# Performance work log

Hardware: AMD Instinct MI355X
Metric: run time of the kernel (lower is better)

The kernel has to match this reference:

```python
import jax, jax.numpy as jnp
import numpy as np

N_NODES = 100000
N_EDGES = 1200000
D = 64          # node_feat_size
G_FEAT = 128    # graph_feat_size
N_GRAPHS = 256
N_TASKS = 1


def setup_inputs() -> dict:
    key = jax.random.key(0)
    ks = jax.random.split(key, 12)
    node_feats = jax.random.normal(ks[0], (N_NODES, D), dtype=jnp.float32)
    edge_feats = jax.random.normal(ks[1], (N_EDGES, 8), dtype=jnp.float32)
    src = jax.random.randint(ks[2], (N_EDGES,), 0, N_NODES, dtype=jnp.int64 if jax.config.read('jax_enable_x64') else jnp.int32)
    dst = jax.random.randint(ks[3], (N_EDGES,), 0, N_NODES, dtype=src.dtype)
    graph_ids = jnp.sort(jax.random.randint(ks[4], (N_NODES,), 0, N_GRAPHS, dtype=src.dtype))
    s = 1.0 / np.sqrt(D)
    W_gcn = jax.random.uniform(ks[5], (D, D), minval=-s, maxval=s, dtype=jnp.float32)
    b_gcn = jnp.zeros((D,), jnp.float32)
    W_res = jax.random.uniform(ks[6], (D, D), minval=-s, maxval=s, dtype=jnp.float32)
    b_res = jnp.zeros((D,), jnp.float32)
    W_in = jax.random.uniform(ks[7], (D, D), minval=-s, maxval=s, dtype=jnp.float32)
    b_in = jnp.zeros((D,), jnp.float32)
    W_out = jax.random.uniform(ks[8], (D, G_FEAT), minval=-s, maxval=s, dtype=jnp.float32)
    b_out = jnp.zeros((G_FEAT,), jnp.float32)
    sp = 1.0 / np.sqrt(G_FEAT)
    W_pred = jax.random.uniform(ks[9], (G_FEAT, N_TASKS), minval=-sp, maxval=sp, dtype=jnp.float32)
    b_pred = jnp.zeros((N_TASKS,), jnp.float32)
    return dict(node_feats=node_feats, edge_feats=edge_feats, src=src, dst=dst,
                graph_ids=graph_ids, W_gcn=W_gcn, b_gcn=b_gcn, W_res=W_res, b_res=b_res,
                W_in=W_in, b_in=b_in, W_out=W_out, b_out=b_out, W_pred=W_pred, b_pred=b_pred)


def reference(node_feats, edge_feats, src, dst, graph_ids,
              W_gcn, b_gcn, W_res, b_res, W_in, b_in, W_out, b_out, W_pred, b_pred):
    # --- GCNLayer (GraphConv norm='none', activation=relu, residual=True) ---
    # message passing: copy src features, sum at dst (no normalization)
    agg = jax.ops.segment_sum(node_feats[src], dst, num_segments=N_NODES)  # [N, D]
    h = jax.nn.relu(agg @ W_gcn + b_gcn)                                   # graph_conv output
    h = h + jax.nn.relu(node_feats @ W_res + b_res)                        # residual branch
    # --- MLPNodeReadout (mode='sum') ---
    h = jax.nn.relu(h @ W_in + b_in)      # [N, D]
    h = h @ W_out + b_out                 # [N, G_FEAT]
    g_feats = jax.ops.segment_sum(h, graph_ids, num_segments=N_GRAPHS)  # [G, G_FEAT]
    # --- predict ---
    out = (g_feats @ W_pred + b_pred).reshape(-1)  # [G * n_tasks]
    return out
```

## Files before the change

kernel.cpp:

```cpp
#include <hip/hip_runtime.h>

typedef __attribute__((ext_vector_type(8))) __bf16 bf16x8;
typedef __attribute__((ext_vector_type(4))) float f32x4;

union Frag { unsigned short u[8]; bf16x8 b; };

__device__ __forceinline__ unsigned short rne_bf16(float x) {
    unsigned int u = __float_as_uint(x);
    return (unsigned short)((u + 0x7fffu + ((u >> 16) & 1u)) >> 16);
}
__device__ __forceinline__ float bf16_to_f(unsigned short h) {
    return __uint_as_float(((unsigned int)h) << 16);
}

#define MFMA16 __builtin_amdgcn_mfma_f32_16x16x32_bf16
#define BCAP 8192

__global__ void prep_kernel(const float* __restrict__ nf,
                            const float* __restrict__ Wg, const float* __restrict__ Wr,
                            const float* __restrict__ Wi, const float* __restrict__ Wo,
                            const float* __restrict__ bo, const float* __restrict__ Wp,
                            const float* __restrict__ bp,
                            unsigned short* __restrict__ nfb,
                            unsigned short* __restrict__ wfrag, float* __restrict__ wfold,
                            float* __restrict__ c0, float* __restrict__ out,
                            int* __restrict__ gcursor, int out_size, int nNodes) {
    int t = blockIdx.x * blockDim.x + threadIdx.x;
    int nth = gridDim.x * blockDim.x;
    const float4* nf4 = (const float4*)nf;
    ushort4* nfb4 = (ushort4*)nfb;
    int nQ = nNodes * 16;
    for (int i = t; i < nQ; i += nth) {
        float4 v = nf4[i];
        ushort4 o;
        o.x = rne_bf16(v.x); o.y = rne_bf16(v.y);
        o.z = rne_bf16(v.z); o.w = rne_bf16(v.w);
        nfb4[i] = o;
    }
    const float* Ws[3] = {Wg, Wr, Wi};
    for (int idx = t; idx < 3 * 2 * 2 * 4 * 64 * 8; idx += nth) {
        int j = idx & 7, lane = (idx >> 3) & 63, nt = (idx >> 9) & 3;
        int kt = (idx >> 11) & 1, part = (idx >> 12) & 1, mat = idx >> 13;
        int k = kt * 32 + ((lane >> 4) << 3) + j;
        int n = nt * 16 + (lane & 15);
        float w = Ws[mat][k * 64 + n];
        unsigned short hi = rne_bf16(w);
        wfrag[idx] = (part == 0) ? hi : rne_bf16(w - bf16_to_f(hi));
    }
    if (t < 64) {
        float s = 0.f;
        for (int j = 0; j < 128; ++j) s += Wo[t * 128 + j] * Wp[j];
        wfold[t] = s;
    }
    if (t == 0) {
        float s = 0.f;
        for (int j = 0; j < 128; ++j) s += bo[j] * Wp[j];
        c0[0] = s;
    }
    if (t < out_size) out[t] = bp[0];
    if (t < 256) gcursor[t] = 0;
}

__global__ __launch_bounds__(256) void bin_kernel(
    const int* __restrict__ src, const int* __restrict__ dst,
    int* __restrict__ gcursor, int* __restrict__ binned, int nE, int nb) {
    __shared__ int lhist[256];
    __shared__ int lbase[256];
    __shared__ int lpos[256];
    int t = threadIdx.x;
    for (int i = t; i < nb; i += 256) { lhist[i] = 0; lpos[i] = 0; }
    __syncthreads();
    int base = blockIdx.x * 4096;
    int end = min(base + 4096, nE);
    for (int e = base + t; e < end; e += 256)
        atomicAdd(&lhist[dst[e] >> 9], 1);
    __syncthreads();
    for (int i = t; i < nb; i += 256) {
        int c = lhist[i];
        lbase[i] = c ? atomicAdd(&gcursor[i], c) : 0;
    }
    __syncthreads();
    for (int e = base + t; e < end; e += 256) {
        int d = dst[e];
        int b = d >> 9;
        int p = atomicAdd(&lpos[b], 1);
        int gp = lbase[b] + p;
        if (gp < BCAP) binned[b * BCAP + gp] = (src[e] << 9) | (d & 511);
    }
}

__global__ __launch_bounds__(1024) void seg_kernel(
    int* __restrict__ binned, const int* __restrict__ gcursor,
    int2* __restrict__ nodeTab, int nNodes) {
    __shared__ int eL[BCAP];
    __shared__ int deg[512];
    __shared__ int scanb[512];
    __shared__ int cur[512];
    const int b = blockIdx.x, t = threadIdx.x;
    const int cnt = min(gcursor[b], BCAP);
    if (t < 512) deg[t] = 0;
    __syncthreads();
    for (int i = t; i < cnt; i += 1024) {
        int p = binned[b * BCAP + i];
        eL[i] = p;
        atomicAdd(&deg[p & 511], 1);
    }
    __syncthreads();
    if (t < 512) scanb[t] = deg[t];
    __syncthreads();
    for (int s = 1; s < 512; s <<= 1) {
        int v = 0;
        if (t < 512 && t >= s) v = scanb[t - s];
        __syncthreads();
        if (t < 512) scanb[t] += v;
        __syncthreads();
    }
    if (t < 512) {
        int excl = scanb[t] - deg[t];
        cur[t] = excl;
        int node = b * 512 + t;
        if (node < nNodes) nodeTab[node] = make_int2(b * BCAP + excl, deg[t]);
    }
    __syncthreads();
    for (int i = t; i < cnt; i += 1024) {
        int p = eL[i];
        int pos = atomicAdd(&cur[p & 511], 1);
        binned[b * BCAP + pos] = p >> 9;
    }
}

__global__ __launch_bounds__(256) void gather_kernel(
    const unsigned short* __restrict__ nfb, const int2* __restrict__ nodeTab,
    const int* __restrict__ srcs, unsigned short* __restrict__ aggb, int nNodes) {
    int wid = blockIdx.x * 4 + (threadIdx.x >> 6);
    if (wid >= nNodes) return;
    int lane = threadIdx.x & 63;
    int half = lane >> 5;
    int cp = lane & 31;
    int2 sd = nodeTab[wid];
    int base = sd.x, d = sd.y;
    const ushort2* nfb2 = (const ushort2*)nfb;
    float ax = 0.f, ay = 0.f;
    int k = half;
    for (; k + 8 <= d; k += 8) {
        int s0 = srcs[base + k],     s1 = srcs[base + k + 2];
        int s2 = srcs[base + k + 4], s3 = srcs[base + k + 6];
        ushort2 v0 = nfb2[(long)s0 * 32 + cp];
        ushort2 v1 = nfb2[(long)s1 * 32 + cp];
        ushort2 v2 = nfb2[(long)s2 * 32 + cp];
        ushort2 v3 = nfb2[(long)s3 * 32 + cp];
        ax += (bf16_to_f(v0.x) + bf16_to_f(v1.x)) + (bf16_to_f(v2.x) + bf16_to_f(v3.x));
        ay += (bf16_to_f(v0.y) + bf16_to_f(v1.y)) + (bf16_to_f(v2.y) + bf16_to_f(v3.y));
    }
    for (; k < d; k += 2) {
        int s = srcs[base + k];
        ushort2 v = nfb2[(long)s * 32 + cp];
        ax += bf16_to_f(v.x); ay += bf16_to_f(v.y);
    }
    ax += __shfl_xor(ax, 32, 64);
    ay += __shfl_xor(ay, 32, 64);
    if (half == 0) {
        ushort2 o; o.x = rne_bf16(ax); o.y = rne_bf16(ay);
        ((ushort2*)aggb)[(long)wid * 32 + cp] = o;
    }
}

__global__ __launch_bounds__(256) void mlp_kernel(
    const unsigned short* __restrict__ aggb, const unsigned short* __restrict__ nfb,
    const int* __restrict__ gids, const unsigned short* __restrict__ wfrag,
    const float* __restrict__ bg, const float* __restrict__ br,
    const float* __restrict__ bi, const float* __restrict__ wfold,
    const float* __restrict__ c0p, float* __restrict__ out, int nTiles) {
    __shared__ float hs_all[4][32 * 68];
    const int wave = threadIdx.x >> 6, lane = threadIdx.x & 63;
    const int wid = blockIdx.x * 4 + wave;
    if (wid >= nTiles) return;
    float* hs = hs_all[wave];
    const int base = wid * 32;
    const int mrow = lane & 15, quad = lane >> 4;

    Frag aA[2][2], aN[2][2];
    #pragma unroll
    for (int rt = 0; rt < 2; ++rt) {
        const unsigned short* rowA = aggb + (long)(base + rt * 16 + mrow) * 64;
        const unsigned short* rowN = nfb  + (long)(base + rt * 16 + mrow) * 64;
        #pragma unroll
        for (int kt = 0; kt < 2; ++kt) {
            aA[rt][kt].b = *(const bf16x8*)(rowA + kt * 32 + quad * 8);
            aN[rt][kt].b = *(const bf16x8*)(rowN + kt * 32 + quad * 8);
        }
    }

    const unsigned short* wl0 = wfrag + lane * 8;
    auto WF = [&](int mat, int part, int kt, int nt) -> bf16x8 {
        return *(const bf16x8*)(wl0 + (size_t)((((mat * 2 + part) * 2 + kt) * 4 + nt) * 64) * 8);
    };

    f32x4 accA[2][4], accR[2][4];
    #pragma unroll
    for (int rt = 0; rt < 2; ++rt)
        #pragma unroll
        for (int nt = 0; nt < 4; ++nt) {
            accA[rt][nt] = (f32x4){0.f, 0.f, 0.f, 0.f};
            accR[rt][nt] = (f32x4){0.f, 0.f, 0.f, 0.f};
        }
    #pragma unroll
    for (int nt = 0; nt < 4; ++nt)
        #pragma unroll
        for (int kt = 0; kt < 2; ++kt) {
            bf16x8 gh = WF(0, 0, kt, nt), gl = WF(0, 1, kt, nt);
            bf16x8 rh = WF(1, 0, kt, nt), rl = WF(1, 1, kt, nt);
            #pragma unroll
            for (int rt = 0; rt < 2; ++rt) {
                accA[rt][nt] = MFMA16(aA[rt][kt].b, gh, accA[rt][nt], 0, 0, 0);
                accA[rt][nt] = MFMA16(aA[rt][kt].b, gl, accA[rt][nt], 0, 0, 0);
                accR[rt][nt] = MFMA16(aN[rt][kt].b, rh, accR[rt][nt], 0, 0, 0);
                accR[rt][nt] = MFMA16(aN[rt][kt].b, rl, accR[rt][nt], 0, 0, 0);
            }
        }

    #pragma unroll
    for (int nt = 0; nt < 4; ++nt) {
        float bgv = bg[nt * 16 + mrow], brv = br[nt * 16 + mrow];
        #pragma unroll
        for (int rt = 0; rt < 2; ++rt)
            #pragma unroll
            for (int r = 0; r < 4; ++r) {
                float h = fmaxf(accA[rt][nt][r] + bgv, 0.f)
                        + fmaxf(accR[rt][nt][r] + brv, 0.f);
                hs[(rt * 16 + quad * 4 + r) * 68 + nt * 16 + mrow] = h;
            }
    }
    __builtin_amdgcn_wave_barrier();

    Frag aH[2][2];
    #pragma unroll
    for (int rt = 0; rt < 2; ++rt)
        #pragma unroll
        for (int kt = 0; kt < 2; ++kt) {
            const float* hp = hs + (rt * 16 + mrow) * 68 + kt * 32 + quad * 8;
            float4 v0 = *(const float4*)hp;
            float4 v1 = *(const float4*)(hp + 4);
            aH[rt][kt].u[0] = rne_bf16(v0.x); aH[rt][kt].u[1] = rne_bf16(v0.y);
            aH[rt][kt].u[2] = rne_bf16(v0.z); aH[rt][kt].u[3] = rne_bf16(v0.w);
            aH[rt][kt].u[4] = rne_bf16(v1.x); aH[rt][kt].u[5] = rne_bf16(v1.y);
            aH[rt][kt].u[6] = rne_bf16(v1.z); aH[rt][kt].u[7] = rne_bf16(v1.w);
        }
    f32x4 accH[2][4];
    #pragma unroll
    for (int rt = 0; rt < 2; ++rt)
        #pragma unroll
        for (int nt = 0; nt < 4; ++nt)
            accH[rt][nt] = (f32x4){0.f, 0.f, 0.f, 0.f};
    #pragma unroll
    for (int nt = 0; nt < 4; ++nt)
        #pragma unroll
        for (int kt = 0; kt < 2; ++kt) {
            bf16x8 ih = WF(2, 0, kt, nt), il = WF(2, 1, kt, nt);
            #pragma unroll
            for (int rt = 0; rt < 2; ++rt) {
                accH[rt][nt] = MFMA16(aH[rt][kt].b, ih, accH[rt][nt], 0, 0, 0);
                accH[rt][nt] = MFMA16(aH[rt][kt].b, il, accH[rt][nt], 0, 0, 0);
            }
        }

    float p[2][4];
    #pragma unroll
    for (int rt = 0; rt < 2; ++rt)
        #pragma unroll
        for (int r = 0; r < 4; ++r) p[rt][r] = 0.f;
    #pragma unroll
    for (int nt = 0; nt < 4; ++nt) {
        float biv = bi[nt * 16 + mrow], wfv = wfold[nt * 16 + mrow];
        #pragma unroll
        for (int rt = 0; rt < 2; ++rt)
            #pragma unroll
            for (int r = 0; r < 4; ++r)
                p[rt][r] += fmaxf(accH[rt][nt][r] + biv, 0.f) * wfv;
    }
    #pragma unroll
    for (int m = 1; m <= 8; m <<= 1)
        #pragma unroll
        for (int rt = 0; rt < 2; ++rt)
            #pragma unroll
            for (int r = 0; r < 4; ++r)
                p[rt][r] += __shfl_xor(p[rt][r], m, 64);
    const float c0 = c0p[0];
    #pragma unroll
    for (int rt = 0; rt < 2; ++rt)
        #pragma unroll
        for (int r = 0; r < 4; ++r) p[rt][r] += c0;

    int gself = gids[base + (lane & 31)];
    int g0 = __shfl(gself, 0, 64);
    if (__all(gself == g0)) {
        float pv = 0.f;
        if (mrow == 0) {
            #pragma unroll
            for (int rt = 0; rt < 2; ++rt)
                #pragma unroll
                for (int r = 0; r < 4; ++r) pv += p[rt][r];
        }
        pv += __shfl_xor(pv, 16, 64);
        pv += __shfl_xor(pv, 32, 64);
        if (lane == 0) atomicAdd(out + g0, pv);
    } else if (mrow == 0) {
        #pragma unroll
        for (int rt = 0; rt < 2; ++rt)
            #pragma unroll
            for (int r = 0; r < 4; ++r)
                atomicAdd(out + gids[base + rt * 16 + quad * 4 + r], p[rt][r]);
    }
}

extern "C" void kernel_launch(void* const* d_in, const int* in_sizes, int n_in,
                              void* d_out, int out_size, void* d_ws, size_t ws_size,
                              hipStream_t stream) {
    const float* node_feats = (const float*)d_in[0];
    const int* src  = (const int*)d_in[2];
    const int* dst  = (const int*)d_in[3];
    const int* gids = (const int*)d_in[4];
    const float* Wg = (const float*)d_in[5];
    const float* bg = (const float*)d_in[6];
    const float* Wr = (const float*)d_in[7];
    const float* br = (const float*)d_in[8];
    const float* Wi = (const float*)d_in[9];
    const float* bi = (const float*)d_in[10];
    const float* Wo = (const float*)d_in[11];
    const float* bo = (const float*)d_in[12];
    const float* Wp = (const float*)d_in[13];
    const float* bp = (const float*)d_in[14];
    float* out = (float*)d_out;

    const int nNodes = in_sizes[0] / 64;
    const int nE = in_sizes[2];
    const int nb = (nNodes + 511) / 512;

    int* gcursor = (int*)d_ws;
    int* binned  = gcursor + 256;
    int2* nodeTab = (int2*)(binned + (size_t)nb * BCAP);
    unsigned short* nfb  = (unsigned short*)(nodeTab + nNodes);
    unsigned short* aggb = nfb + (size_t)nNodes * 64;
    unsigned short* wfrag = aggb + (size_t)nNodes * 64;
    float* wfold = (float*)(wfrag + 3 * 2 * 2 * 4 * 64 * 8);
    float* c0 = wfold + 64;

    prep_kernel<<<2048, 256, 0, stream>>>(node_feats, Wg, Wr, Wi, Wo, bo, Wp, bp,
                                          nfb, wfrag, wfold, c0, out, gcursor,
                                          out_size, nNodes);
    bin_kernel<<<(nE + 4095) / 4096, 256, 0, stream>>>(src, dst, gcursor, binned, nE, nb);
    seg_kernel<<<nb, 1024, 0, stream>>>(binned, gcursor, nodeTab, nNodes);
    gather_kernel<<<(nNodes + 3) / 4, 256, 0, stream>>>(nfb, nodeTab, binned, aggb, nNodes);

    const int nTiles = (nNodes + 31) / 32;
    mlp_kernel<<<(nTiles + 3) / 4, 256, 0, stream>>>(aggb, nfb, gids, wfrag,
        bg, br, bi, wfold, c0, out, nTiles);
}
```

Before: 232.2 us.

## Fuse prep and binning into one kernel with finer 128-node buckets

Merges the bf16 conversion/weight prep kernel with the edge binning kernel into a single launch, with separate block ranges doing each job concurrently. Bucket size drops from 512 to 128 nodes (782 buckets, capacity 2048 each), so seg_kernel runs more, smaller 256-thread blocks with a shorter scan and less LDS. The cursor reset moves to a memset. This removes a launch and lets binning overlap with the conversion, but the smaller bucket capacity leaves less slack for overflow and the prep side now runs on fewer blocks.

```diff
diff --git a/kernel.cpp b/kernel.cpp
--- a/kernel.cpp
+++ b/kernel.cpp
@@ -14,23 +14,53 @@
 }
 
 #define MFMA16 __builtin_amdgcn_mfma_f32_16x16x32_bf16
-#define BCAP 8192
-
-__global__ void prep_kernel(const float* __restrict__ nf,
-                            const float* __restrict__ Wg, const float* __restrict__ Wr,
-                            const float* __restrict__ Wi, const float* __restrict__ Wo,
-                            const float* __restrict__ bo, const float* __restrict__ Wp,
-                            const float* __restrict__ bp,
-                            unsigned short* __restrict__ nfb,
-                            unsigned short* __restrict__ wfrag, float* __restrict__ wfold,
-                            float* __restrict__ c0, float* __restrict__ out,
-                            int* __restrict__ gcursor, int out_size, int nNodes) {
-    int t = blockIdx.x * blockDim.x + threadIdx.x;
-    int nth = gridDim.x * blockDim.x;
+#define BSH 7
+#define BNODES 128
+#define BCAP 2048
+#define BINCHUNK 4096
+#define NWFRAG (3 * 2 * 2 * 4 * 64 * 8)
+
+__global__ __launch_bounds__(256) void prepbin_kernel(
+    const float* __restrict__ nf, const int* __restrict__ src,
+    const int* __restrict__ dst,
+    const float* __restrict__ Wg, const float* __restrict__ Wr,
+    const float* __restrict__ Wi, const float* __restrict__ Wo,
+    const float* __restrict__ bo, const float* __restrict__ Wp,
+    const float* __restrict__ bp,
+    unsigned short* __restrict__ nfb, unsigned short* __restrict__ wfrag,
+    float* __restrict__ wfold, float* __restrict__ c0, float* __restrict__ out,
+    int* __restrict__ gcursor, int* __restrict__ binned,
+    int nBin, int nE, int nb, int out_size, int nNodes) {
+    __shared__ int lhist[800], lbase[800], lpos[800];
+    const int t = threadIdx.x;
+    if ((int)blockIdx.x < nBin) {
+        for (int i = t; i < nb; i += 256) { lhist[i] = 0; lpos[i] = 0; }
+        __syncthreads();
+        const int e0 = blockIdx.x * BINCHUNK;
+        const int e1 = min(e0 + BINCHUNK, nE);
+        for (int e = e0 + t; e < e1; e += 256)
+            atomicAdd(&lhist[dst[e] >> BSH], 1);
+        __syncthreads();
+        for (int i = t; i < nb; i += 256) {
+            int c = lhist[i];
+            lbase[i] = c ? atomicAdd(&gcursor[i], c) : 0;
+        }
+        __syncthreads();
+        for (int e = e0 + t; e < e1; e += 256) {
+            int d = dst[e];
+            int bkt = d >> BSH;
+            int p = atomicAdd(&lpos[bkt], 1);
+            int gp = lbase[bkt] + p;
+            if (gp < BCAP) binned[bkt * BCAP + gp] = (src[e] << BSH) | (d & (BNODES - 1));
+        }
+        return;
+    }
+    const int tp = ((int)blockIdx.x - nBin) * 256 + t;
+    const int nth = ((int)gridDim.x - nBin) * 256;
     const float4* nf4 = (const float4*)nf;
     ushort4* nfb4 = (ushort4*)nfb;
-    int nQ = nNodes * 16;
-    for (int i = t; i < nQ; i += nth) {
+    const int nQ = nNodes * 16;
+    for (int i = tp; i < nQ; i += nth) {
         float4 v = nf4[i];
         ushort4 o;
         o.x = rne_bf16(v.x); o.y = rne_bf16(v.y);
@@ -38,7 +68,7 @@
         nfb4[i] = o;
     }
     const float* Ws[3] = {Wg, Wr, Wi};
-    for (int idx = t; idx < 3 * 2 * 2 * 4 * 64 * 8; idx += nth) {
+    for (int idx = tp; idx < NWFRAG; idx += nth) {
         int j = idx & 7, lane = (idx >> 3) & 63, nt = (idx >> 9) & 3;
         int kt = (idx >> 11) & 1, part = (idx >> 12) & 1, mat = idx >> 13;
         int k = kt * 32 + ((lane >> 4) << 3) + j;
@@ -47,85 +77,55 @@
         unsigned short hi = rne_bf16(w);
         wfrag[idx] = (part == 0) ? hi : rne_bf16(w - bf16_to_f(hi));
     }
-    if (t < 64) {
+    if (tp < 64) {
         float s = 0.f;
-        for (int j = 0; j < 128; ++j) s += Wo[t * 128 + j] * Wp[j];
-        wfold[t] = s;
-    }
-    if (t == 0) {
+        for (int j = 0; j < 128; ++j) s += Wo[tp * 128 + j] * Wp[j];
+        wfold[tp] = s;
+    }
+    if (tp == 0) {
         float s = 0.f;
         for (int j = 0; j < 128; ++j) s += bo[j] * Wp[j];
         c0[0] = s;
     }
-    if (t < out_size) out[t] = bp[0];
-    if (t < 256) gcursor[t] = 0;
-}
-
-__global__ __launch_bounds__(256) void bin_kernel(
-    const int* __restrict__ src, const int* __restrict__ dst,
-    int* __restrict__ gcursor, int* __restrict__ binned, int nE, int nb) {
-    __shared__ int lhist[256];
-    __shared__ int lbase[256];
-    __shared__ int lpos[256];
-    int t = threadIdx.x;
-    for (int i = t; i < nb; i += 256) { lhist[i] = 0; lpos[i] = 0; }
-    __syncthreads();
-    int base = blockIdx.x * 4096;
-    int end = min(base + 4096, nE);
-    for (int e = base + t; e < end; e += 256)
-        atomicAdd(&lhist[dst[e] >> 9], 1);
-    __syncthreads();
-    for (int i = t; i < nb; i += 256) {
-        int c = lhist[i];
-        lbase[i] = c ? atomicAdd(&gcursor[i], c) : 0;
-    }
-    __syncthreads();
-    for (int e = base + t; e < end; e += 256) {
-        int d = dst[e];
-        int b = d >> 9;
-        int p = atomicAdd(&lpos[b], 1);
-        int gp = lbase[b] + p;
-        if (gp < BCAP) binned[b * BCAP + gp] = (src[e] << 9) | (d & 511);
-    }
-}
-
-__global__ __launch_bounds__(1024) void seg_kernel(
+    if (tp < out_size) out[tp] = bp[0];
+}
+
+__global__ __launch_bounds__(256) void seg_kernel(
     int* __restrict__ binned, const int* __restrict__ gcursor,
     int2* __restrict__ nodeTab, int nNodes) {
     __shared__ int eL[BCAP];
-    __shared__ int deg[512];
-    __shared__ int scanb[512];
-    __shared__ int cur[512];
+    __shared__ int deg[BNODES], sc[BNODES], cur[BNODES];
     const int b = blockIdx.x, t = threadIdx.x;
     const int cnt = min(gcursor[b], BCAP);
-    if (t < 512) deg[t] = 0;
+    if (t < BNODES) deg[t] = 0;
     __syncthreads();
-    for (int i = t; i < cnt; i += 1024) {
+    for (int i = t; i < cnt; i += 256) {
         int p = binned[b * BCAP + i];
         eL[i] = p;
-        atomicAdd(&deg[p & 511], 1);
+        atomicAdd(&deg[p & (BNODES - 1)], 1);
     }
     __syncthreads();
-    if (t < 512) scanb[t] = deg[t];
+    if (t < BNODES) sc[t] = deg[t];
     __syncthreads();
-    for (int s = 1; s < 512; s <<= 1) {
+    #pragma unroll
+    for (int s = 1; s < BNODES; s <<= 1) {
         int v = 0;
-        if (t < 512 && t >= s) v = scanb[t - s];
-        __syncthreads();
-        if (t < 512) scanb[t] += v;
-        __syncthreads();
-    }
-    if (t < 512) {
-        int excl = scanb[t] - deg[t];
+        if (t < BNODES && t >= s) v = sc[t - s];
+        __syncthreads();
+        if (t < BNODES) sc[t] += v;
+        __syncthreads();
+    }
+    if (t < BNODES) {
+        int excl = sc[t] - deg[t];
         cur[t] = excl;
-        int node = b * 512 + t;
+        int node = b * BNODES + t;
         if (node < nNodes) nodeTab[node] = make_int2(b * BCAP + excl, deg[t]);
     }
     __syncthreads();
-    for (int i = t; i < cnt; i += 1024) {
+    for (int i = t; i < cnt; i += 256) {
         int p = eL[i];
-        int pos = atomicAdd(&cur[p & 511], 1);
-        binned[b * BCAP + pos] = p >> 9;
+        int pos = atomicAdd(&cur[p & (BNODES - 1)], 1);
+        binned[b * BCAP + pos] = p >> BSH;
     }
 }
 
@@ -334,22 +334,26 @@
 
     const int nNodes = in_sizes[0] / 64;
     const int nE = in_sizes[2];
-    const int nb = (nNodes + 511) / 512;
+    const int nb = (nNodes + BNODES - 1) / BNODES;
 
     int* gcursor = (int*)d_ws;
-    int* binned  = gcursor + 256;
+    int* binned  = gcursor + 1024;
     int2* nodeTab = (int2*)(binned + (size_t)nb * BCAP);
     unsigned short* nfb  = (unsigned short*)(nodeTab + nNodes);
     unsigned short* aggb = nfb + (size_t)nNodes * 64;
     unsigned short* wfrag = aggb + (size_t)nNodes * 64;
-    float* wfold = (float*)(wfrag + 3 * 2 * 2 * 4 * 64 * 8);
+    float* wfold = (float*)(wfrag + NWFRAG);
     float* c0 = wfold + 64;
 
-    prep_kernel<<<2048, 256, 0, stream>>>(node_feats, Wg, Wr, Wi, Wo, bo, Wp, bp,
-                                          nfb, wfrag, wfold, c0, out, gcursor,
-                                          out_size, nNodes);
-    bin_kernel<<<(nE + 4095) / 4096, 256, 0, stream>>>(src, dst, gcursor, binned, nE, nb);
-    seg_kernel<<<nb, 1024, 0, stream>>>(binned, gcursor, nodeTab, nNodes);
+    hipMemsetAsync(gcursor, 0, 1024 * sizeof(int), stream);
+
+    const int nBin = (nE + BINCHUNK - 1) / BINCHUNK;
+    prepbin_kernel<<<nBin + 512, 256, 0, stream>>>(
+        node_feats, src, dst, Wg, Wr, Wi, Wo, bo, Wp, bp,
+        nfb, wfrag, wfold, c0, out, gcursor, binned,
+        nBin, nE, nb, out_size, nNodes);
+
+    seg_kernel<<<nb, 256, 0, stream>>>(binned, gcursor, nodeTab, nNodes);
     gather_kernel<<<(nNodes + 3) / 4, 256, 0, stream>>>(nfb, nodeTab, binned, aggb, nNodes);
 
     const int nTiles = (nNodes + 31) / 32;
```

Result: no change. 233.4 us (+0.5%).
